# Performance work log

Measured on AMD Instinct MI355X. Metric: run time of the kernel, lower is better.

Reference implementation:

```python
import jax, jax.numpy as jnp
import numpy as np

NUM_RECORDS = 10000
NUM_CODES = 128
CODE_DIM = 128
BATCH = 32
NUM_POINTS = 4096
EPS = 1e-16


def setup_inputs() -> dict:
    key = jax.random.key(0)
    k1, k2, k3, k4 = jax.random.split(key, 4)
    indices = jax.random.randint(k1, (BATCH,), 0, NUM_RECORDS)
    query_points = jax.random.uniform(k2, (BATCH, NUM_POINTS, 3), dtype=jnp.float32) - 0.5
    codes_position = jax.random.uniform(k3, (NUM_RECORDS, NUM_CODES, 3), dtype=jnp.float32) - 0.5
    codes = jax.random.normal(k4, (NUM_RECORDS, NUM_CODES, CODE_DIM), dtype=jnp.float32) * 0.01
    return {
        "indices": indices,
        "query_points": query_points,
        "codes_position": codes_position,
        "codes": codes,
        "dist_scale": 2,
    }


def reference(indices, query_points, codes_position, codes, dist_scale):
    # Gather per-record code clouds: (B, C, 3) and (B, C, D)
    batch_pos = codes_position[indices]
    batch_codes = codes[indices]
    # Pairwise squared distance: (B, P, C)
    diff = query_points[:, :, None, :] - batch_pos[:, None, :, :]
    square_dist = jnp.sum(diff * diff, axis=-1) + EPS
    # Inverse-distance weights: 1 / sqrt(d)^s, normalized over codes
    weight = 1.0 / jnp.sqrt(square_dist) ** dist_scale
    weight = weight / jnp.sum(weight, axis=-1, keepdims=True)
    # Weighted sum of codes: (B, P, C) @ (B, C, D) -> (B, P, D)
    query_codes = jnp.einsum('bpc,bcd->bpd', weight, batch_codes)
    return (query_codes, square_dist, weight)
```

## Files before the change

kernel.cpp:

```cpp
#include <hip/hip_runtime.h>
#include <hip/hip_bf16.h>

#define NB 32
#define NP 4096
#define NC 128
#define ND 128
#define TP 128
#define EPSV 1e-16f

typedef __attribute__((ext_vector_type(8))) short short8;
typedef __attribute__((ext_vector_type(4))) float f32x4;

__device__ __forceinline__ unsigned short f2bf(float f) {
  __hip_bfloat16 h = __float2bfloat16(f);
  return *reinterpret_cast<unsigned short*>(&h);
}

__device__ __forceinline__ int swz(int row, int kbyte) {
  return (row * 256 + kbyte) ^ ((row & 7) << 4);
}

__global__ void cc_pre(const int* __restrict__ indices,
                       const float* __restrict__ codes,
                       unsigned char* __restrict__ ws) {
  const int b = blockIdx.x >> 3;
  const int chunk = blockIdx.x & 7;
  const int rec = indices[b];
  const float* cb = codes + (size_t)rec * (NC * ND);
  unsigned char* wb = ws + (size_t)b * (NC * ND * 2);
  const int tid = threadIdx.x;
  const int d = chunk * 16 + (tid & 15);
  const int c0 = (tid >> 4) * 8;
  short8 v;
  #pragma unroll
  for (int j = 0; j < 8; ++j)
    v[j] = (short)f2bf(cb[(size_t)(c0 + j) * ND + d]);
  *(short8*)(wb + swz(d, c0 * 2)) = v;
}

template<bool PRE>
__global__ __launch_bounds__(256, 2) void cc_main(
    const int* __restrict__ indices,
    const float* __restrict__ qp,
    const float* __restrict__ cpos,
    const float* __restrict__ codes,
    const void* __restrict__ dsp,
    const unsigned char* __restrict__ wsc,
    float* __restrict__ out_qc,
    float* __restrict__ out_sq,
    float* __restrict__ out_wt) {
  __shared__ __align__(16) unsigned char wT[TP * NC * 2];
  __shared__ __align__(16) unsigned char cT[ND * NC * 2];

  const int tid = threadIdx.x;
  const int lane = tid & 63;
  const int wv = tid >> 6;
  const int g = lane >> 4;
  const int l16 = lane & 15;
  const int c0 = l16 * 8;
  const int b = blockIdx.x >> 5;
  const int p0 = (blockIdx.x & 31) * TP;
  const int rec = indices[b];

  const int si = ((const int*)dsp)[0];
  const float sv = (si > 0 && si < 1000) ? (float)si : ((const float*)dsp)[0];

  const float* pb = cpos + ((size_t)rec * NC + c0) * 3;
  float px[8], py[8], pz[8];
  #pragma unroll
  for (int j = 0; j < 8; ++j) {
    px[j] = pb[j * 3 + 0]; py[j] = pb[j * 3 + 1]; pz[j] = pb[j * 3 + 2];
  }

  const size_t rowbase = (size_t)b * NP + p0;
  float qx[8], qy[8], qz[8];
  #pragma unroll
  for (int it = 0; it < 8; ++it) {
    const int p = it * 16 + wv * 4 + g;
    const float* q = qp + (rowbase + p) * 3;
    qx[it] = q[0]; qy[it] = q[1]; qz[it] = q[2];
  }

  if (PRE) {
    const unsigned char* src = wsc + (size_t)b * (NC * ND * 2);
    #pragma unroll
    for (int it = 0; it < 8; ++it) {
      const int off = (wv * 8 + it) * 1024;
      __builtin_amdgcn_global_load_lds(
          (const __attribute__((address_space(1))) void*)(src + off + lane * 16),
          (__attribute__((address_space(3))) void*)(cT + off),
          16, 0, 0);
    }
  } else {
    const float* cb = codes + (size_t)rec * (NC * ND);
    #pragma unroll
    for (int it = 0; it < 16; ++it) {
      int i = tid * 4 + it * 1024;
      float4 v = *reinterpret_cast<const float4*>(cb + i);
      int c = i >> 7, d0 = i & 127;
      float vv[4] = {v.x, v.y, v.z, v.w};
      #pragma unroll
      for (int j = 0; j < 4; ++j)
        *(unsigned short*)(cT + swz(d0 + j, c * 2)) = f2bf(vv[j]);
    }
  }

  const bool s2 = (sv == 2.0f);
  #pragma unroll
  for (int it = 0; it < 8; ++it) {
    const int p = it * 16 + wv * 4 + g;
    float dd[8], wu[8];
    #pragma unroll
    for (int j = 0; j < 8; ++j) {
      const float dx = qx[it] - px[j], dy = qy[it] - py[j], dz = qz[it] - pz[j];
      dd[j] = fmaf(dx, dx, fmaf(dy, dy, dz * dz)) + EPSV;
    }
    if (s2) {
      #pragma unroll
      for (int j = 0; j < 8; ++j) wu[j] = __builtin_amdgcn_rcpf(dd[j]);
    } else {
      #pragma unroll
      for (int j = 0; j < 8; ++j) wu[j] = __powf(dd[j], -0.5f * sv);
    }
    float s = ((wu[0] + wu[1]) + (wu[2] + wu[3])) + ((wu[4] + wu[5]) + (wu[6] + wu[7]));
    s += __shfl_xor(s, 1); s += __shfl_xor(s, 2);
    s += __shfl_xor(s, 4); s += __shfl_xor(s, 8);
    const float inv = __builtin_amdgcn_rcpf(s);

    f32x4 dlo, dhi, wlo, whi;
    #pragma unroll
    for (int j = 0; j < 4; ++j) {
      dlo[j] = dd[j]; dhi[j] = dd[j + 4];
      wlo[j] = wu[j] * inv; whi[j] = wu[j + 4] * inv;
    }
    const size_t rb = (rowbase + p) * (size_t)NC + c0;
    *(f32x4*)(out_sq + rb) = dlo;
    *(f32x4*)(out_sq + rb + 4) = dhi;
    *(f32x4*)(out_wt + rb) = wlo;
    *(f32x4*)(out_wt + rb + 4) = whi;

    short8 w8;
    #pragma unroll
    for (int j = 0; j < 4; ++j) { w8[j] = (short)f2bf(wlo[j]); w8[j + 4] = (short)f2bf(whi[j]); }
    *(short8*)(wT + swz(p, c0 * 2)) = w8;
  }

  __syncthreads();

  const int kg = lane >> 4;
  f32x4 acc[2][8];
  #pragma unroll
  for (int pi = 0; pi < 2; ++pi)
    #pragma unroll
    for (int mi = 0; mi < 8; ++mi)
      acc[pi][mi] = (f32x4){0.f, 0.f, 0.f, 0.f};

  const int pr0 = wv * 32 + l16;
  #pragma unroll
  for (int kk = 0; kk < NC; kk += 32) {
    const int kb = (kk + kg * 8) * 2;
    const short8 b0 = *(const short8*)(wT + swz(pr0, kb));
    const short8 b1 = *(const short8*)(wT + swz(pr0 + 16, kb));
    #pragma unroll
    for (int mi = 0; mi < 8; ++mi) {
      const short8 a8 = *(const short8*)(cT + swz(mi * 16 + l16, kb));
      acc[0][mi] = __builtin_amdgcn_mfma_f32_16x16x32_bf16(a8, b0, acc[0][mi], 0, 0, 0);
      acc[1][mi] = __builtin_amdgcn_mfma_f32_16x16x32_bf16(a8, b1, acc[1][mi], 0, 0, 0);
    }
  }

  float* q0 = out_qc + (rowbase + pr0) * (size_t)ND + kg * 4;
  float* q1 = out_qc + (rowbase + pr0 + 16) * (size_t)ND + kg * 4;
  #pragma unroll
  for (int mi = 0; mi < 8; ++mi) {
    *(f32x4*)(q0 + mi * 16) = acc[0][mi];
    *(f32x4*)(q1 + mi * 16) = acc[1][mi];
  }

  (void)codes;
}

extern "C" void kernel_launch(void* const* d_in, const int* in_sizes, int n_in,
                              void* d_out, int out_size, void* d_ws, size_t ws_size,
                              hipStream_t stream) {
  const int* indices = (const int*)d_in[0];
  const float* qp = (const float*)d_in[1];
  const float* cpos = (const float*)d_in[2];
  const float* codes = (const float*)d_in[3];
  const void* dsp = d_in[4];

  float* out = (float*)d_out;
  float* qc = out;
  float* sq = qc + (size_t)NB * NP * ND;
  float* wt = sq + (size_t)NB * NP * NC;

  const size_t ws_need = (size_t)NB * NC * ND * 2;
  dim3 grid(NB * (NP / TP));
  if (ws_size >= ws_need) {
    cc_pre<<<dim3(NB * 8), dim3(256), 0, stream>>>(indices, codes, (unsigned char*)d_ws);
    cc_main<true><<<grid, 256, 0, stream>>>(indices, qp, cpos, codes, dsp,
                                            (const unsigned char*)d_ws, qc, sq, wt);
  } else {
    cc_main<false><<<grid, 256, 0, stream>>>(indices, qp, cpos, codes, dsp,
                                             nullptr, qc, sq, wt);
  }
}
```

Measured before the change: 45.33 us.

## Recompute weights in MFMA fragment layout instead of staging them through LDS

The 32 KB LDS buffer holding bf16 weights is removed. Each lane now recomputes the distances and unnormalized weights it needs directly in the MFMA B-operand layout, using code positions staged in LDS and a per-point inverse sum shared through LDS. Launch bounds are raised from 2 to 4 blocks per SM so that the smaller LDS footprint allows more occupancy. The cost is doing the distance and reciprocal math twice, plus more register pressure under the tighter launch bound.

```diff
diff --git a/kernel.cpp b/kernel.cpp
--- a/kernel.cpp
+++ b/kernel.cpp
@@ -39,7 +39,7 @@
 }
 
 template<bool PRE>
-__global__ __launch_bounds__(256, 2) void cc_main(
+__global__ __launch_bounds__(256, 4) void cc_main(
     const int* __restrict__ indices,
     const float* __restrict__ qp,
     const float* __restrict__ cpos,
@@ -49,8 +49,9 @@
     float* __restrict__ out_qc,
     float* __restrict__ out_sq,
     float* __restrict__ out_wt) {
-  __shared__ __align__(16) unsigned char wT[TP * NC * 2];
   __shared__ __align__(16) unsigned char cT[ND * NC * 2];
+  __shared__ __align__(16) float pos4[NC][4];
+  __shared__ float isum[TP];
 
   const int tid = threadIdx.x;
   const int lane = tid & 63;
@@ -65,6 +66,12 @@
   const int si = ((const int*)dsp)[0];
   const float sv = (si > 0 && si < 1000) ? (float)si : ((const float*)dsp)[0];
 
+  if (tid < NC) {
+    const float* cp = cpos + ((size_t)rec * NC + tid) * 3;
+    pos4[tid][0] = cp[0]; pos4[tid][1] = cp[1]; pos4[tid][2] = cp[2];
+    pos4[tid][3] = 0.f;
+  }
+
   const float* pb = cpos + ((size_t)rec * NC + c0) * 3;
   float px[8], py[8], pz[8];
   #pragma unroll
@@ -80,6 +87,12 @@
     const float* q = qp + (rowbase + p) * 3;
     qx[it] = q[0]; qy[it] = q[1]; qz[it] = q[2];
   }
+
+  const int pr0 = wv * 32 + l16;
+  const float* qq0 = qp + (rowbase + pr0) * 3;
+  const float* qq1 = qp + (rowbase + pr0 + 16) * 3;
+  const float q0x = qq0[0], q0y = qq0[1], q0z = qq0[2];
+  const float q1x = qq1[0], q1y = qq1[1], q1z = qq1[2];
 
   if (PRE) {
     const unsigned char* src = wsc + (size_t)b * (NC * ND * 2);
@@ -126,6 +139,7 @@
     s += __shfl_xor(s, 1); s += __shfl_xor(s, 2);
     s += __shfl_xor(s, 4); s += __shfl_xor(s, 8);
     const float inv = __builtin_amdgcn_rcpf(s);
+    if (l16 == 0) isum[p] = inv;
 
     f32x4 dlo, dhi, wlo, whi;
     #pragma unroll
@@ -138,16 +152,13 @@
     *(f32x4*)(out_sq + rb + 4) = dhi;
     *(f32x4*)(out_wt + rb) = wlo;
     *(f32x4*)(out_wt + rb + 4) = whi;
-
-    short8 w8;
-    #pragma unroll
-    for (int j = 0; j < 4; ++j) { w8[j] = (short)f2bf(wlo[j]); w8[j + 4] = (short)f2bf(whi[j]); }
-    *(short8*)(wT + swz(p, c0 * 2)) = w8;
   }
 
   __syncthreads();
 
   const int kg = lane >> 4;
+  const float inv0 = isum[pr0];
+  const float inv1 = isum[pr0 + 16];
   f32x4 acc[2][8];
   #pragma unroll
   for (int pi = 0; pi < 2; ++pi)
@@ -155,29 +166,39 @@
     for (int mi = 0; mi < 8; ++mi)
       acc[pi][mi] = (f32x4){0.f, 0.f, 0.f, 0.f};
 
-  const int pr0 = wv * 32 + l16;
-  #pragma unroll
-  for (int kk = 0; kk < NC; kk += 32) {
-    const int kb = (kk + kg * 8) * 2;
-    const short8 b0 = *(const short8*)(wT + swz(pr0, kb));
-    const short8 b1 = *(const short8*)(wT + swz(pr0 + 16, kb));
+  #pragma unroll
+  for (int kk = 0; kk < 4; ++kk) {
+    const int cbase = kk * 32 + kg * 8;
+    short8 bf0, bf1;
+    #pragma unroll
+    for (int j = 0; j < 8; ++j) {
+      const float4 pc = *(const float4*)&pos4[cbase + j][0];
+      float dx = q0x - pc.x, dy = q0y - pc.y, dz = q0z - pc.z;
+      const float d0 = fmaf(dx, dx, fmaf(dy, dy, dz * dz)) + EPSV;
+      dx = q1x - pc.x; dy = q1y - pc.y; dz = q1z - pc.z;
+      const float d1 = fmaf(dx, dx, fmaf(dy, dy, dz * dz)) + EPSV;
+      float w0, w1;
+      if (s2) { w0 = __builtin_amdgcn_rcpf(d0); w1 = __builtin_amdgcn_rcpf(d1); }
+      else    { w0 = __powf(d0, -0.5f * sv);    w1 = __powf(d1, -0.5f * sv); }
+      bf0[j] = (short)f2bf(w0 * inv0);
+      bf1[j] = (short)f2bf(w1 * inv1);
+    }
+    const int kb = cbase * 2;
     #pragma unroll
     for (int mi = 0; mi < 8; ++mi) {
       const short8 a8 = *(const short8*)(cT + swz(mi * 16 + l16, kb));
-      acc[0][mi] = __builtin_amdgcn_mfma_f32_16x16x32_bf16(a8, b0, acc[0][mi], 0, 0, 0);
-      acc[1][mi] = __builtin_amdgcn_mfma_f32_16x16x32_bf16(a8, b1, acc[1][mi], 0, 0, 0);
-    }
-  }
-
-  float* q0 = out_qc + (rowbase + pr0) * (size_t)ND + kg * 4;
-  float* q1 = out_qc + (rowbase + pr0 + 16) * (size_t)ND + kg * 4;
+      acc[0][mi] = __builtin_amdgcn_mfma_f32_16x16x32_bf16(a8, bf0, acc[0][mi], 0, 0, 0);
+      acc[1][mi] = __builtin_amdgcn_mfma_f32_16x16x32_bf16(a8, bf1, acc[1][mi], 0, 0, 0);
+    }
+  }
+
+  float* o0 = out_qc + (rowbase + pr0) * (size_t)ND + kg * 4;
+  float* o1 = out_qc + (rowbase + pr0 + 16) * (size_t)ND + kg * 4;
   #pragma unroll
   for (int mi = 0; mi < 8; ++mi) {
-    *(f32x4*)(q0 + mi * 16) = acc[0][mi];
-    *(f32x4*)(q1 + mi * 16) = acc[1][mi];
-  }
-
-  (void)codes;
+    *(f32x4*)(o0 + mi * 16) = acc[0][mi];
+    *(f32x4*)(o1 + mi * 16) = acc[1][mi];
+  }
 }
 
 extern "C" void kernel_launch(void* const* d_in, const int* in_sizes, int n_in,
```

Result: slower. 47.84 us (+5.5%).

## Make weight tiles wave-local and interleave code columns for coalesced stores

Applied to the files above, without the earlier changes.

Each wave now computes weights for exactly the 32 query rows it later consumes in the MFMA stage, writing them into its own slice of shared memory. That removes the cross-wave dependency on the weight tile. Code-position ownership per lane is remapped to 4 codes in each half of the row, so 16 lanes write contiguous 256-byte segments of the distance and weight outputs. The block barrier moves before the distance computation and now only guards the codes tile load, which may reduce overlap of that load with the weight math.

```diff
diff --git a/kernel.cpp b/kernel.cpp
--- a/kernel.cpp
+++ b/kernel.cpp
@@ -9,6 +9,7 @@
 #define EPSV 1e-16f
 
 typedef __attribute__((ext_vector_type(8))) short short8;
+typedef __attribute__((ext_vector_type(4))) short short4v;
 typedef __attribute__((ext_vector_type(4))) float f32x4;
 
 __device__ __forceinline__ unsigned short f2bf(float f) {
@@ -49,37 +50,21 @@
     float* __restrict__ out_qc,
     float* __restrict__ out_sq,
     float* __restrict__ out_wt) {
+  __shared__ __align__(16) unsigned char cT[ND * NC * 2];
   __shared__ __align__(16) unsigned char wT[TP * NC * 2];
-  __shared__ __align__(16) unsigned char cT[ND * NC * 2];
 
   const int tid = threadIdx.x;
   const int lane = tid & 63;
   const int wv = tid >> 6;
   const int g = lane >> 4;
   const int l16 = lane & 15;
-  const int c0 = l16 * 8;
   const int b = blockIdx.x >> 5;
   const int p0 = (blockIdx.x & 31) * TP;
   const int rec = indices[b];
+  unsigned char* wTw = wT + wv * 8192;
 
   const int si = ((const int*)dsp)[0];
   const float sv = (si > 0 && si < 1000) ? (float)si : ((const float*)dsp)[0];
-
-  const float* pb = cpos + ((size_t)rec * NC + c0) * 3;
-  float px[8], py[8], pz[8];
-  #pragma unroll
-  for (int j = 0; j < 8; ++j) {
-    px[j] = pb[j * 3 + 0]; py[j] = pb[j * 3 + 1]; pz[j] = pb[j * 3 + 2];
-  }
-
-  const size_t rowbase = (size_t)b * NP + p0;
-  float qx[8], qy[8], qz[8];
-  #pragma unroll
-  for (int it = 0; it < 8; ++it) {
-    const int p = it * 16 + wv * 4 + g;
-    const float* q = qp + (rowbase + p) * 3;
-    qx[it] = q[0]; qy[it] = q[1]; qz[it] = q[2];
-  }
 
   if (PRE) {
     const unsigned char* src = wsc + (size_t)b * (NC * ND * 2);
@@ -105,10 +90,30 @@
     }
   }
 
+  const float* pb0 = cpos + ((size_t)rec * NC + l16 * 4) * 3;
+  const float* pb1 = cpos + ((size_t)rec * NC + 64 + l16 * 4) * 3;
+  float px[8], py[8], pz[8];
+  #pragma unroll
+  for (int j = 0; j < 4; ++j) {
+    px[j] = pb0[j * 3 + 0]; py[j] = pb0[j * 3 + 1]; pz[j] = pb0[j * 3 + 2];
+    px[j + 4] = pb1[j * 3 + 0]; py[j + 4] = pb1[j * 3 + 1]; pz[j + 4] = pb1[j * 3 + 2];
+  }
+
+  const size_t rowbase = (size_t)b * NP + p0;
+  float qx[8], qy[8], qz[8];
+  #pragma unroll
+  for (int it = 0; it < 8; ++it) {
+    const int p = wv * 32 + it * 4 + g;
+    const float* q = qp + (rowbase + p) * 3;
+    qx[it] = q[0]; qy[it] = q[1]; qz[it] = q[2];
+  }
+
+  __syncthreads();
+
   const bool s2 = (sv == 2.0f);
   #pragma unroll
   for (int it = 0; it < 8; ++it) {
-    const int p = it * 16 + wv * 4 + g;
+    const int p = wv * 32 + it * 4 + g;
     float dd[8], wu[8];
     #pragma unroll
     for (int j = 0; j < 8; ++j) {
@@ -133,21 +138,26 @@
       dlo[j] = dd[j]; dhi[j] = dd[j + 4];
       wlo[j] = wu[j] * inv; whi[j] = wu[j + 4] * inv;
     }
-    const size_t rb = (rowbase + p) * (size_t)NC + c0;
-    *(f32x4*)(out_sq + rb) = dlo;
-    *(f32x4*)(out_sq + rb + 4) = dhi;
-    *(f32x4*)(out_wt + rb) = wlo;
-    *(f32x4*)(out_wt + rb + 4) = whi;
-
-    short8 w8;
-    #pragma unroll
-    for (int j = 0; j < 4; ++j) { w8[j] = (short)f2bf(wlo[j]); w8[j + 4] = (short)f2bf(whi[j]); }
-    *(short8*)(wT + swz(p, c0 * 2)) = w8;
-  }
-
-  __syncthreads();
+    const size_t rb = (rowbase + p) * (size_t)NC;
+    *(f32x4*)(out_sq + rb + l16 * 4) = dlo;
+    *(f32x4*)(out_sq + rb + 64 + l16 * 4) = dhi;
+    *(f32x4*)(out_wt + rb + l16 * 4) = wlo;
+    *(f32x4*)(out_wt + rb + 64 + l16 * 4) = whi;
+
+    short4v wbl, wbh;
+    #pragma unroll
+    for (int j = 0; j < 4; ++j) {
+      wbl[j] = (short)f2bf(wlo[j]);
+      wbh[j] = (short)f2bf(whi[j]);
+    }
+    const int r = it * 4 + g;
+    *(short4v*)(wTw + swz(r, l16 * 8)) = wbl;
+    *(short4v*)(wTw + swz(r, 128 + l16 * 8)) = wbh;
+  }
+
 
   const int kg = lane >> 4;
+  const int pr0 = wv * 32 + l16;
   f32x4 acc[2][8];
   #pragma unroll
   for (int pi = 0; pi < 2; ++pi)
@@ -155,12 +165,11 @@
     for (int mi = 0; mi < 8; ++mi)
       acc[pi][mi] = (f32x4){0.f, 0.f, 0.f, 0.f};
 
-  const int pr0 = wv * 32 + l16;
   #pragma unroll
   for (int kk = 0; kk < NC; kk += 32) {
     const int kb = (kk + kg * 8) * 2;
-    const short8 b0 = *(const short8*)(wT + swz(pr0, kb));
-    const short8 b1 = *(const short8*)(wT + swz(pr0 + 16, kb));
+    const short8 b0 = *(const short8*)(wTw + swz(l16, kb));
+    const short8 b1 = *(const short8*)(wTw + swz(l16 + 16, kb));
     #pragma unroll
     for (int mi = 0; mi < 8; ++mi) {
       const short8 a8 = *(const short8*)(cT + swz(mi * 16 + l16, kb));
@@ -169,12 +178,12 @@
     }
   }
 
-  float* q0 = out_qc + (rowbase + pr0) * (size_t)ND + kg * 4;
-  float* q1 = out_qc + (rowbase + pr0 + 16) * (size_t)ND + kg * 4;
+  float* o0 = out_qc + (rowbase + pr0) * (size_t)ND + kg * 4;
+  float* o1 = out_qc + (rowbase + pr0 + 16) * (size_t)ND + kg * 4;
   #pragma unroll
   for (int mi = 0; mi < 8; ++mi) {
-    *(f32x4*)(q0 + mi * 16) = acc[0][mi];
-    *(f32x4*)(q1 + mi * 16) = acc[1][mi];
+    *(f32x4*)(o0 + mi * 16) = acc[0][mi];
+    *(f32x4*)(o1 + mi * 16) = acc[1][mi];
   }
 
   (void)codes;
```

Result: no change. 44.53 us (-1.8%).
